# Kernel tuning notes

Hardware: AMD Instinct MI355X
Metric: run time of the kernel (lower is better)

The kernel has to match this reference:

```python
import jax, jax.numpy as jnp
import numpy as np

D = 96           # fine dense grid edge
SF = 2           # scale_factor
S = SF ** 3      # sub-voxels per coarse voxel
DS = D // SF     # coarse grid edge
C = 64           # in_channels
OUT = 64         # out_channels


def setup_inputs() -> dict:
    key = jax.random.key(0)
    k1, k2 = jax.random.split(key)
    N = D ** 3
    # dense grid ijk in canonical (lexicographic) order -> sorted in_index holds
    r = jnp.arange(N, dtype=jnp.int32)
    ijk = jnp.stack([r // (D * D), (r // D) % D, r % D], axis=-1)  # [N,3] int32
    in_data = jax.random.normal(k1, (N, C), dtype=jnp.float32)
    w_out = jax.random.normal(k2, (S * C, OUT), dtype=jnp.float32) * (1.0 / np.sqrt(S * C))
    return {"in_data": in_data, "ijk": ijk, "w_out": w_out}


def reference(in_data, ijk, w_out):
    ijk = ijk.astype(jnp.int32)
    down_ijk = ijk // SF                      # floor division (coords >= 0)
    local = ijk - down_ijk * SF               # [N,3] in [0, SF)
    # local flat index: i*SF^2 + j*SF + k
    local_index = local[:, 0] * (SF * SF) + local[:, 1] * SF + local[:, 2]
    # canonical index into dense coarsened grid (matches ijk_to_index on dense grid)
    down_index = down_ijk[:, 0] * (DS * DS) + down_ijk[:, 1] * DS + down_ijk[:, 2]
    flat_idx = down_index * S + local_index    # [N], unique by construction
    # scatter_add into pre-zeroed buffer (space-to-depth reorg)
    flat_target = jnp.zeros((DS ** 3 * S, C), dtype=in_data.dtype)
    flat_target = flat_target.at[flat_idx].add(in_data)
    down_data = flat_target.reshape(DS ** 3, S * C)   # [Nd, S*C]
    out = down_data @ w_out                            # [Nd, OUT]
    return out
```

## Files before the change

### kernel.cpp

```cpp
#include <hip/hip_runtime.h>
#include <hip/hip_bf16.h>

#define DD 96
#define DSS 48
#define CCH 64
#define OUTC 64
#define KDIM 512
#define MTILE 48
#define LDS_ROW 136

typedef __bf16 bf16x8 __attribute__((ext_vector_type(8)));
typedef float f32x4 __attribute__((ext_vector_type(4)));
typedef unsigned int u32;

__device__ __forceinline__ unsigned short f2bf(float f) {
    u32 u = __builtin_bit_cast(u32, f);
    u += 0x7FFFu + ((u >> 16) & 1u);
    return (unsigned short)(u >> 16);
}

__global__ void wprep_kernel(const float* __restrict__ w, unsigned short* __restrict__ wf) {
    int id = blockIdx.x * 256 + threadIdx.x;
    if (id >= 4 * 16 * 64 * 8) return;
    int j  = id & 7;
    int L  = (id >> 3) & 63;
    int ks = (id >> 9) & 15;
    int t  = id >> 13;
    int k  = ks * 32 + (L >> 4) * 8 + j;
    int n  = t * 16 + (L & 15);
    wf[id] = f2bf(w[k * OUTC + n]);
}

template <bool USE_WS>
__global__ __launch_bounds__(256, 4) void ds_gemm_kernel(
    const float* __restrict__ in,
    const float* __restrict__ w,
    const unsigned short* __restrict__ wf,
    float* __restrict__ out)
{
    __shared__ unsigned short Ash[2][MTILE * LDS_ROW];

    const int b    = blockIdx.x;
    const int di   = b / DSS;
    const int dj   = b % DSS;
    const int tid  = threadIdx.x;
    const int wv   = tid >> 6;
    const int lane = tid & 63;
    const int q    = lane >> 4;
    const int mrow = lane & 15;

    f32x4 acc[3];
    acc[0] = f32x4{0.f, 0.f, 0.f, 0.f};
    acc[1] = f32x4{0.f, 0.f, 0.f, 0.f};
    acc[2] = f32x4{0.f, 0.f, 0.f, 0.f};

    f32x4 vreg[6];

    auto loadchunk = [&](int c) {
        const int li = c >> 1, lj = c & 1;
        const f32x4* seg4 = (const f32x4*)(in +
            (size_t)(((2 * di + li) * (DD * DD) + (2 * dj + lj) * DD) * CCH));
#pragma unroll
        for (int it = 0; it < 6; it++) vreg[it] = seg4[it * 256 + tid];
    };

    auto writechunk = [&](int buf) {
#pragma unroll
        for (int it = 0; it < 6; it++) {
            const int f = it * 256 + tid;
            const int e = f * 4;
            const int row = e >> 7;
            const int col = e & 127;
            u32 p0 = ((u32)f2bf(vreg[it].y) << 16) | f2bf(vreg[it].x);
            u32 p1 = ((u32)f2bf(vreg[it].w) << 16) | f2bf(vreg[it].z);
            u32 pk[2] = {p0, p1};
            __builtin_memcpy((void*)&Ash[buf][row * LDS_ROW + col], pk, 8);
        }
    };

    auto compute = [&](int c, int buf) {
        bf16x8 bfr[4];
        if (USE_WS) {
#pragma unroll
            for (int ks = 0; ks < 4; ks++) {
                bf16x8 t;
                __builtin_memcpy(&t, &wf[(((wv * 16) + (c * 4 + ks)) * 64 + lane) * 8], 16);
                bfr[ks] = t;
            }
        } else {
#pragma unroll
            for (int ks = 0; ks < 4; ks++) {
                union { bf16x8 v; unsigned short s[8]; } u2;
#pragma unroll
                for (int j = 0; j < 8; j++)
                    u2.s[j] = f2bf(w[((c * 4 + ks) * 32 + q * 8 + j) * OUTC + wv * 16 + (lane & 15)]);
                bfr[ks] = u2.v;
            }
        }
#pragma unroll
        for (int ks = 0; ks < 4; ks++) {
            const int koff = ks * 32 + q * 8;
#pragma unroll
            for (int mt = 0; mt < 3; mt++) {
                bf16x8 af;
                __builtin_memcpy(&af, &Ash[buf][(mt * 16 + mrow) * LDS_ROW + koff], 16);
                acc[mt] = __builtin_amdgcn_mfma_f32_16x16x32_bf16(af, bfr[ks], acc[mt], 0, 0, 0);
            }
        }
    };

    loadchunk(0); writechunk(0);
    __syncthreads();
    loadchunk(1); compute(0, 0); writechunk(1);
    __syncthreads();
    loadchunk(2); compute(1, 1); writechunk(0);
    __syncthreads();
    loadchunk(3); compute(2, 0); writechunk(1);
    __syncthreads();
    compute(3, 1);

    const int ncol = wv * 16 + (lane & 15);
    const int rbase = q * 4;
#pragma unroll
    for (int mt = 0; mt < 3; mt++) {
#pragma unroll
        for (int r = 0; r < 4; r++) {
            const int m = b * MTILE + mt * 16 + rbase + r;
            out[m * OUTC + ncol] = acc[mt][r];
        }
    }
}

extern "C" void kernel_launch(void* const* d_in, const int* in_sizes, int n_in,
                              void* d_out, int out_size, void* d_ws, size_t ws_size,
                              hipStream_t stream) {
    const float* in = (const float*)d_in[0];
    const float* w  = (const float*)d_in[2];
    float* out = (float*)d_out;

    if (ws_size >= 65536) {
        wprep_kernel<<<128, 256, 0, stream>>>(w, (unsigned short*)d_ws);
        ds_gemm_kernel<true><<<DSS * DSS, 256, 0, stream>>>(
            in, w, (const unsigned short*)d_ws, out);
    } else {
        ds_gemm_kernel<false><<<DSS * DSS, 256, 0, stream>>>(in, w, nullptr, out);
    }
}
```

Measured before the change: 323.4 us.

## Load A fragments directly from global into registers, drop LDS staging

Replaces the LDS double-buffered staging of the input tile with direct per-lane global loads of fp32 A fragments, converted to bf16 in registers and fed straight to MFMA. The work split changes from 4 waves each owning an N-slice of the output to 3 waves each owning a 16-row M-slice across all 64 output columns. B fragments and the next A fragment are prefetched one k-step ahead in registers. This removes shared-memory writes, reads and block barriers, at the cost of each lane issuing strided 32-byte global reads and all waves reloading the full weight fragments.

```diff
diff --git a/kernel.cpp b/kernel.cpp
--- a/kernel.cpp
+++ b/kernel.cpp
@@ -5,23 +5,22 @@
 #define DSS 48
 #define CCH 64
 #define OUTC 64
-#define KDIM 512
-#define MTILE 48
-#define LDS_ROW 136
 
+typedef __bf16 bf16_t;
 typedef __bf16 bf16x8 __attribute__((ext_vector_type(8)));
 typedef float f32x4 __attribute__((ext_vector_type(4)));
 typedef unsigned int u32;
+typedef unsigned short u16;
 
-__device__ __forceinline__ unsigned short f2bf(float f) {
+__device__ __forceinline__ u16 f2bf(float f) {
     u32 u = __builtin_bit_cast(u32, f);
     u += 0x7FFFu + ((u >> 16) & 1u);
-    return (unsigned short)(u >> 16);
+    return (u16)(u >> 16);
 }
 
-__global__ void wprep_kernel(const float* __restrict__ w, unsigned short* __restrict__ wf) {
+__global__ void wprep_kernel(const float* __restrict__ w, u16* __restrict__ wf) {
     int id = blockIdx.x * 256 + threadIdx.x;
-    if (id >= 4 * 16 * 64 * 8) return;
+    if (id >= 16 * 64 * 8 * 4) return;
     int j  = id & 7;
     int L  = (id >> 3) & 63;
     int ks = (id >> 9) & 15;
@@ -32,103 +31,89 @@
 }
 
 template <bool USE_WS>
-__global__ __launch_bounds__(256, 4) void ds_gemm_kernel(
+__global__ __launch_bounds__(192) void ds_gemm_kernel(
     const float* __restrict__ in,
     const float* __restrict__ w,
-    const unsigned short* __restrict__ wf,
+    const u16* __restrict__ wf,
     float* __restrict__ out)
 {
-    __shared__ unsigned short Ash[2][MTILE * LDS_ROW];
-
-    const int b    = blockIdx.x;
-    const int di   = b / DSS;
-    const int dj   = b % DSS;
     const int tid  = threadIdx.x;
     const int wv   = tid >> 6;
     const int lane = tid & 63;
     const int q    = lane >> 4;
     const int mrow = lane & 15;
+    const int b    = blockIdx.x;
+    const int di   = b / DSS;
+    const int dj   = b % DSS;
+    const int dkb  = wv * 16;
 
-    f32x4 acc[3];
-    acc[0] = f32x4{0.f, 0.f, 0.f, 0.f};
-    acc[1] = f32x4{0.f, 0.f, 0.f, 0.f};
-    acc[2] = f32x4{0.f, 0.f, 0.f, 0.f};
+    const float* base[4];
+#pragma unroll
+    for (int c = 0; c < 4; c++) {
+        const int li = c >> 1, lj = c & 1;
+        base[c] = in + (size_t)((2 * di + li) * (DD * DD) + (2 * dj + lj) * DD) * CCH;
+    }
+    const int laneoff = 2 * (dkb + mrow) * CCH + q * 8;
 
-    f32x4 vreg[6];
-
-    auto loadchunk = [&](int c) {
-        const int li = c >> 1, lj = c & 1;
-        const f32x4* seg4 = (const f32x4*)(in +
-            (size_t)(((2 * di + li) * (DD * DD) + (2 * dj + lj) * DD) * CCH));
+    auto aaddr = [&](int ks) -> const f32x4* {
+        return (const f32x4*)(base[ks >> 2] + laneoff
+                              + ((ks >> 1) & 1) * CCH + (ks & 1) * 32);
+    };
+    auto bload = [&](int ks, int nt) -> bf16x8 {
+        bf16x8 t;
+        if (USE_WS) {
+            __builtin_memcpy(&t, wf + (size_t)(((nt * 16 + ks) * 64) + lane) * 8, 16);
+        } else {
+            union { bf16x8 v; u16 s[8]; } u2;
 #pragma unroll
-        for (int it = 0; it < 6; it++) vreg[it] = seg4[it * 256 + tid];
+            for (int j = 0; j < 8; j++)
+                u2.s[j] = f2bf(w[(ks * 32 + q * 8 + j) * OUTC + nt * 16 + mrow]);
+            t = u2.v;
+        }
+        return t;
     };
 
-    auto writechunk = [&](int buf) {
+    f32x4 acc[4];
 #pragma unroll
-        for (int it = 0; it < 6; it++) {
-            const int f = it * 256 + tid;
-            const int e = f * 4;
-            const int row = e >> 7;
-            const int col = e & 127;
-            u32 p0 = ((u32)f2bf(vreg[it].y) << 16) | f2bf(vreg[it].x);
-            u32 p1 = ((u32)f2bf(vreg[it].w) << 16) | f2bf(vreg[it].z);
-            u32 pk[2] = {p0, p1};
-            __builtin_memcpy((void*)&Ash[buf][row * LDS_ROW + col], pk, 8);
+    for (int nt = 0; nt < 4; nt++) acc[nt] = f32x4{0.f, 0.f, 0.f, 0.f};
+
+    f32x4 ar0 = aaddr(0)[0];
+    f32x4 ar1 = aaddr(0)[1];
+    bf16x8 bcur[4];
+#pragma unroll
+    for (int nt = 0; nt < 4; nt++) bcur[nt] = bload(0, nt);
+
+#pragma unroll
+    for (int ks = 0; ks < 16; ks++) {
+        f32x4 nr0, nr1;
+        bf16x8 bnext[4];
+        if (ks < 15) {
+            nr0 = aaddr(ks + 1)[0];
+            nr1 = aaddr(ks + 1)[1];
+#pragma unroll
+            for (int nt = 0; nt < 4; nt++) bnext[nt] = bload(ks + 1, nt);
         }
-    };
-
-    auto compute = [&](int c, int buf) {
-        bf16x8 bfr[4];
-        if (USE_WS) {
+        union { bf16x8 v; bf16_t e[8]; } af;
+        af.e[0] = (bf16_t)ar0.x; af.e[1] = (bf16_t)ar0.y;
+        af.e[2] = (bf16_t)ar0.z; af.e[3] = (bf16_t)ar0.w;
+        af.e[4] = (bf16_t)ar1.x; af.e[5] = (bf16_t)ar1.y;
+        af.e[6] = (bf16_t)ar1.z; af.e[7] = (bf16_t)ar1.w;
 #pragma unroll
-            for (int ks = 0; ks < 4; ks++) {
-                bf16x8 t;
-                __builtin_memcpy(&t, &wf[(((wv * 16) + (c * 4 + ks)) * 64 + lane) * 8], 16);
-                bfr[ks] = t;
-            }
-        } else {
+        for (int nt = 0; nt < 4; nt++)
+            acc[nt] = __builtin_amdgcn_mfma_f32_16x16x32_bf16(af.v, bcur[nt], acc[nt], 0, 0, 0);
+        if (ks < 15) {
+            ar0 = nr0; ar1 = nr1;
 #pragma unroll
-            for (int ks = 0; ks < 4; ks++) {
-                union { bf16x8 v; unsigned short s[8]; } u2;
-#pragma unroll
-                for (int j = 0; j < 8; j++)
-                    u2.s[j] = f2bf(w[((c * 4 + ks) * 32 + q * 8 + j) * OUTC + wv * 16 + (lane & 15)]);
-                bfr[ks] = u2.v;
-            }
-        }
-#pragma unroll
-        for (int ks = 0; ks < 4; ks++) {
-            const int koff = ks * 32 + q * 8;
-#pragma unroll
-            for (int mt = 0; mt < 3; mt++) {
-                bf16x8 af;
-                __builtin_memcpy(&af, &Ash[buf][(mt * 16 + mrow) * LDS_ROW + koff], 16);
-                acc[mt] = __builtin_amdgcn_mfma_f32_16x16x32_bf16(af, bfr[ks], acc[mt], 0, 0, 0);
-            }
-        }
-    };
-
-    loadchunk(0); writechunk(0);
-    __syncthreads();
-    loadchunk(1); compute(0, 0); writechunk(1);
-    __syncthreads();
-    loadchunk(2); compute(1, 1); writechunk(0);
-    __syncthreads();
-    loadchunk(3); compute(2, 0); writechunk(1);
-    __syncthreads();
-    compute(3, 1);
-
-    const int ncol = wv * 16 + (lane & 15);
-    const int rbase = q * 4;
-#pragma unroll
-    for (int mt = 0; mt < 3; mt++) {
-#pragma unroll
-        for (int r = 0; r < 4; r++) {
-            const int m = b * MTILE + mt * 16 + rbase + r;
-            out[m * OUTC + ncol] = acc[mt][r];
+            for (int nt = 0; nt < 4; nt++) bcur[nt] = bnext[nt];
         }
     }
+
+    const int mb = b * 48 + dkb + q * 4;
+#pragma unroll
+    for (int nt = 0; nt < 4; nt++)
+#pragma unroll
+        for (int r = 0; r < 4; r++)
+            out[(size_t)(mb + r) * OUTC + nt * 16 + mrow] = acc[nt][r];
 }
 
 extern "C" void kernel_launch(void* const* d_in, const int* in_sizes, int n_in,
@@ -139,10 +124,10 @@
     float* out = (float*)d_out;
 
     if (ws_size >= 65536) {
-        wprep_kernel<<<128, 256, 0, stream>>>(w, (unsigned short*)d_ws);
-        ds_gemm_kernel<true><<<DSS * DSS, 256, 0, stream>>>(
-            in, w, (const unsigned short*)d_ws, out);
+        wprep_kernel<<<128, 256, 0, stream>>>(w, (u16*)d_ws);
+        ds_gemm_kernel<true><<<DSS * DSS, 192, 0, stream>>>(
+            in, w, (const u16*)d_ws, out);
     } else {
-        ds_gemm_kernel<false><<<DSS * DSS, 256, 0, stream>>>(in, w, nullptr, out);
+        ds_gemm_kernel<false><<<DSS * DSS, 192, 0, stream>>>(in, w, nullptr, out);
     }
 }
```

New measurement: 331.1 us. +2.4%, slower.
